# Kernel tuning notes

Measured on AMD Instinct MI355X. Metric: run time of the kernel, lower is better.

## Reference

```python
import jax, jax.numpy as jnp
import numpy as np

K, A, DIM = 1024, 16384, 512


def setup_inputs() -> dict:
    key = jax.random.key(0)
    ks = jax.random.split(key, 8)
    B, H, W = 2048, 8, 8
    z_t = jax.random.randint(ks[0], (B, H, W), 0, K, dtype=jnp.int64)
    z_tp1 = jax.random.randint(ks[1], (B, H, W), 0, K, dtype=jnp.int64)
    embed_w = jax.random.normal(ks[2], (K, DIM), dtype=jnp.float32) * 0.02
    # MLP: Linear(2*dim -> dim), GELU, Linear(dim -> dim)
    lim1 = 1.0 / np.sqrt(2 * DIM)
    w1 = jax.random.uniform(ks[3], (2 * DIM, DIM), minval=-lim1, maxval=lim1, dtype=jnp.float32)
    b1 = jax.random.uniform(ks[4], (DIM,), minval=-lim1, maxval=lim1, dtype=jnp.float32)
    lim2 = 1.0 / np.sqrt(DIM)
    w2 = jax.random.uniform(ks[5], (DIM, DIM), minval=-lim2, maxval=lim2, dtype=jnp.float32)
    b2 = jax.random.uniform(ks[6], (DIM,), minval=-lim2, maxval=lim2, dtype=jnp.float32)
    codebook_w = jax.random.normal(ks[7], (A, DIM), dtype=jnp.float32) * 0.02
    return {"z_t": z_t, "z_tp1": z_tp1, "embed_w": embed_w, "w1": w1, "b1": b1,
            "w2": w2, "b2": b2, "codebook_w": codebook_w}


def reference(z_t, z_tp1, embed_w, w1, b1, w2, b2, codebook_w):
    B = z_t.shape[0]
    # embed int code grids and mean-pool over H*W tokens -> [B, dim]
    e_t = embed_w[z_t.reshape(B, -1)].mean(axis=1)
    e_tp1 = embed_w[z_tp1.reshape(B, -1)].mean(axis=1)
    h = jnp.concatenate([e_t, e_tp1], axis=-1)          # [B, 2*dim]
    h = jax.nn.gelu(h @ w1 + b1, approximate=False)
    e = h @ w2 + b2                                      # [B, dim]
    # VQ: squared L2 distance to each code, argmin, gather
    d2 = (jnp.sum(e * e, axis=1, keepdims=True)
          - 2.0 * e @ codebook_w.T
          + jnp.sum(codebook_w * codebook_w, axis=1)[None, :])  # [B, A]
    ids = jnp.argmin(d2, axis=1)                         # [B]
    q = codebook_w[ids]                                  # [B, dim]
    return ids, q
```

## Files before the change

### kernel.cpp

```cpp
#include <hip/hip_runtime.h>
#include <hip/hip_bf16.h>

#define TOK 64
#define DIMC 512

typedef __attribute__((ext_vector_type(8))) short v8s;
typedef __attribute__((ext_vector_type(4))) float v4f;

#define MFMA16 __builtin_amdgcn_mfma_f32_16x16x32_bf16

__device__ __forceinline__ unsigned int f2ord(float f) {
  unsigned int u = __float_as_uint(f);
  return (u & 0x80000000u) ? ~u : (u | 0x80000000u);
}

__device__ __forceinline__ float gelu_exact(float x) {
  return 0.5f * x * (1.0f + erff(x * 0.70710678118654752440f));
}

__device__ __forceinline__ unsigned short f2bf(float x) {
  unsigned int u = __float_as_uint(x);
  return (unsigned short)((u + 0x7FFFu + ((u >> 16) & 1u)) >> 16);
}
__device__ __forceinline__ float bf2f(unsigned short h) {
  return __uint_as_float((unsigned int)h << 16);
}

__device__ __forceinline__ void gl2lds16(const void* g, void* l) {
  __builtin_amdgcn_global_load_lds((const __attribute__((address_space(1))) void*)g,
                                   (__attribute__((address_space(3))) void*)l,
                                   16, 0, 0);
}

__global__ __launch_bounds__(256) void k_prep(
    const int* __restrict__ zt, const int* __restrict__ ztp,
    const float* __restrict__ emb,
    unsigned short* __restrict__ hh, unsigned short* __restrict__ hl,
    unsigned long long* __restrict__ rowmin,
    const float* __restrict__ w1, unsigned short* __restrict__ w1th,
    unsigned short* __restrict__ w1tl,
    const float* __restrict__ w2, unsigned short* __restrict__ w2th,
    unsigned short* __restrict__ w2tl,
    const float* __restrict__ cb, unsigned short* __restrict__ ch,
    unsigned short* __restrict__ cl, float* __restrict__ cnorm) {
  __shared__ int codes[128];
  __shared__ float tbuf[32][33];
  const int bid = blockIdx.x;
  const int tid = threadIdx.x;

  if (bid < 2048) {
    const int b = bid;
    if (tid < 64) codes[tid] = zt[b * TOK + tid];
    else if (tid < 128) codes[tid] = ztp[b * TOK + (tid - 64)];
    if (tid == 0) rowmin[b] = 0xFFFFFFFFFFFFFFFFull;
    __syncthreads();
    const int half = tid >> 7;
    const int c4 = tid & 127;
    const float4* emb4 = (const float4*)emb;
    float4 s = make_float4(0.f, 0.f, 0.f, 0.f);
    #pragma unroll 8
    for (int t = 0; t < TOK; t++) {
      const int code = codes[half * TOK + t];
      const float4 v = emb4[code * 128 + c4];
      s.x += v.x; s.y += v.y; s.z += v.z; s.w += v.w;
    }
    const float inv = 1.0f / 64.0f;
    float f[4] = {s.x * inv, s.y * inv, s.z * inv, s.w * inv};
    unsigned short hi[4], lo[4];
    #pragma unroll
    for (int i = 0; i < 4; i++) {
      hi[i] = f2bf(f[i]);
      lo[i] = f2bf(f[i] - bf2f(hi[i]));
    }
    const int off = b * 1024 + half * 512 + c4 * 4;
    *(ushort4*)&hh[off] = make_ushort4(hi[0], hi[1], hi[2], hi[3]);
    *(ushort4*)&hl[off] = make_ushort4(lo[0], lo[1], lo[2], lo[3]);
  } else if (bid < 2816) {
    const float* w; unsigned short *wth, *wtl; int Kd, N, k0, n0;
    if (bid < 2560) {
      const int i = bid - 2048;
      w = w1; wth = w1th; wtl = w1tl; Kd = 1024; N = 512;
      k0 = (i & 31) * 32; n0 = (i >> 5) * 32;
    } else {
      const int i = bid - 2560;
      w = w2; wth = w2th; wtl = w2tl; Kd = 512; N = 512;
      k0 = (i & 15) * 32; n0 = (i >> 4) * 32;
    }
    const int c = tid & 31, r = tid >> 5;
    #pragma unroll
    for (int i = 0; i < 4; i++)
      tbuf[r + i * 8][c] = w[(size_t)(k0 + r + i * 8) * N + n0 + c];
    __syncthreads();
    #pragma unroll
    for (int i = 0; i < 4; i++) {
      const float v = tbuf[c][r + i * 8];
      const unsigned short hi = f2bf(v);
      const unsigned short lo = f2bf(v - bf2f(hi));
      wth[(size_t)(n0 + r + i * 8) * Kd + k0 + c] = hi;
      wtl[(size_t)(n0 + r + i * 8) * Kd + k0 + c] = lo;
    }
  } else {
    const int row = (bid - 2816) * 4 + (tid >> 6);
    const int lane = tid & 63;
    const float4* cb4 = (const float4*)cb;
    const float4 va = cb4[row * 128 + lane * 2];
    const float4 vb = cb4[row * 128 + lane * 2 + 1];
    float s = va.x * va.x + va.y * va.y + va.z * va.z + va.w * va.w
            + vb.x * vb.x + vb.y * vb.y + vb.z * vb.z + vb.w * vb.w;
    float f[8] = {va.x, va.y, va.z, va.w, vb.x, vb.y, vb.z, vb.w};
    unsigned short hi[8], lo[8];
    #pragma unroll
    for (int i = 0; i < 8; i++) {
      hi[i] = f2bf(f[i]);
      lo[i] = f2bf(f[i] - bf2f(hi[i]));
    }
    ushort4* chp = (ushort4*)&ch[row * DIMC + lane * 8];
    ushort4* clp = (ushort4*)&cl[row * DIMC + lane * 8];
    chp[0] = make_ushort4(hi[0], hi[1], hi[2], hi[3]);
    chp[1] = make_ushort4(hi[4], hi[5], hi[6], hi[7]);
    clp[0] = make_ushort4(lo[0], lo[1], lo[2], lo[3]);
    clp[1] = make_ushort4(lo[4], lo[5], lo[6], lo[7]);
    #pragma unroll
    for (int off = 32; off > 0; off >>= 1) s += __shfl_down(s, off);
    if (lane == 0) cnorm[row] = s;
  }
}

template <bool GELU>
__global__ __launch_bounds__(256) void k_gemm(const unsigned short* __restrict__ Ah_,
                                              const unsigned short* __restrict__ Al_,
                                              const unsigned short* __restrict__ Bh_,
                                              const unsigned short* __restrict__ Bl_,
                                              const float* __restrict__ bias,
                                              unsigned short* __restrict__ oh,
                                              unsigned short* __restrict__ ol,
                                              int Kd, int N) {
  __shared__ unsigned short AhS[2][2048];
  __shared__ unsigned short AlS[2][2048];
  __shared__ unsigned short BhS[2][4096];
  __shared__ unsigned short BlS[2][4096];

  const int tid = threadIdx.x;
  const int lane = tid & 63;
  const int wid = tid >> 6;
  const int m0 = blockIdx.x * 32;
  const int n0 = blockIdx.y * 64;

  const unsigned short* Ab_h = Ah_ + (size_t)m0 * Kd;
  const unsigned short* Ab_l = Al_ + (size_t)m0 * Kd;
  const unsigned short* Bb_h = Bh_ + (size_t)n0 * Kd;
  const unsigned short* Bb_l = Bl_ + (size_t)n0 * Kd;

  const int srow = lane >> 2;
  const int sk = ((lane & 3) ^ ((lane >> 3) & 3)) * 8;
  const int wm = wid >> 1, wn = wid & 1;
  const int fr = lane & 15;
  const int q = lane >> 4;
  const int fqs = (q ^ ((fr >> 1) & 3)) * 8;

  v4f acc[2];
  acc[0] = (v4f)(0.f);
  acc[1] = (v4f)(0.f);

  auto stage = [&](int b, int k0) {
    #pragma unroll
    for (int u = 0; u < 6; u++) {
      const int i = wid * 6 + u;
      const unsigned short* gs; unsigned short* ls; int slab, seg, rstride;
      if (i < 4)       { gs = Ab_h; ls = AhS[b]; slab = i >> 1;         seg = i & 1;         rstride = 1024; }
      else if (i < 8)  { gs = Ab_l; ls = AlS[b]; slab = (i - 4) >> 1;   seg = (i - 4) & 1;   rstride = 1024; }
      else if (i < 16) { gs = Bb_h; ls = BhS[b]; slab = (i - 8) >> 2;   seg = (i - 8) & 3;   rstride = 2048; }
      else             { gs = Bb_l; ls = BlS[b]; slab = (i - 16) >> 2;  seg = (i - 16) & 3;  rstride = 2048; }
      gl2lds16(gs + (size_t)(seg * 16 + srow) * Kd + k0 + slab * 32 + sk,
               ls + slab * rstride + seg * 512);
    }
  };

  stage(0, 0);
  int cur = 0;
  for (int k0 = 0; k0 < Kd; k0 += 64) {
    __syncthreads();
    if (k0 + 64 < Kd) stage(cur ^ 1, k0 + 64);

    #pragma unroll
    for (int kk = 0; kk < 2; kk++) {
      const int ar = kk * 1024 + (wm * 16 + fr) * 32 + fqs;
      const v8s ah = *(const v8s*)&AhS[cur][ar];
      const v8s al = *(const v8s*)&AlS[cur][ar];
      #pragma unroll
      for (int nt = 0; nt < 2; nt++) {
        const int br = kk * 2048 + (wn * 32 + nt * 16 + fr) * 32 + fqs;
        const v8s bh = *(const v8s*)&BhS[cur][br];
        const v8s bl = *(const v8s*)&BlS[cur][br];
        acc[nt] = MFMA16(ah, bh, acc[nt], 0, 0, 0);
        acc[nt] = MFMA16(ah, bl, acc[nt], 0, 0, 0);
        acc[nt] = MFMA16(al, bh, acc[nt], 0, 0, 0);
      }
    }
    cur ^= 1;
  }

  const int col16 = lane & 15;
  #pragma unroll
  for (int nt = 0; nt < 2; nt++) {
    const int col = n0 + wn * 32 + nt * 16 + col16;
    const float bv = bias[col];
    #pragma unroll
    for (int reg = 0; reg < 4; reg++) {
      const int row = m0 + wm * 16 + q * 4 + reg;
      float v = acc[nt][reg] + bv;
      if (GELU) v = gelu_exact(v);
      const unsigned short hi = f2bf(v);
      oh[(size_t)row * N + col] = hi;
      ol[(size_t)row * N + col] = f2bf(v - bf2f(hi));
    }
  }
}

__global__ __launch_bounds__(512, 2) void k_vq(const unsigned short* __restrict__ eh,
                                               const unsigned short* __restrict__ el,
                                               const unsigned short* __restrict__ ch,
                                               const unsigned short* __restrict__ cl,
                                               const float* __restrict__ cnorm,
                                               unsigned long long* __restrict__ rowmin) {
  __shared__ unsigned short lds[2 * 32768];

  const int tid = threadIdx.x;
  const int lane = tid & 63;
  const int wid = tid >> 6;
  const int bid = blockIdx.x;
  const int x = (bid >> 3) & 7;
  const int y = (((bid >> 6) & 7) << 3) | (bid & 7);
  const int r0 = x * 256;
  const int c0 = y * 256;

  const unsigned short* ehB = eh + (size_t)r0 * DIMC;
  const unsigned short* elB = el + (size_t)r0 * DIMC;
  const unsigned short* chB = ch + (size_t)c0 * DIMC;
  const unsigned short* clB = cl + (size_t)c0 * DIMC;

  const int srow = lane >> 2;
  const int sk = ((lane & 3) ^ ((lane >> 3) & 3)) * 8;
  const int wm = wid >> 1;
  const int wn = wid & 1;
  const int fr = lane & 15;
  const int q = lane >> 4;
  const int fqs = (q ^ ((fr >> 1) & 3)) * 8;

  v4f acc[4][8];
  #pragma unroll
  for (int i = 0; i < 4; i++)
    #pragma unroll
    for (int jj = 0; jj < 8; jj++) acc[i][jj] = (v4f)(0.f);

  const unsigned short* gp[8];
  int lo_[8];
  #pragma unroll
  for (int u = 0; u < 8; u++) {
    const int i = wid * 8 + u;
    const unsigned short* gs; int off, rbase;
    if (i < 16)      { gs = ehB; off = 0;     rbase = i * 16; }
    else if (i < 32) { gs = elB; off = 8192;  rbase = (i - 16) * 16; }
    else if (i < 48) { gs = chB; off = 16384; rbase = (i - 32) * 16; }
    else             { gs = clB; off = 24576; rbase = (i - 48) * 16; }
    gp[u] = gs + (size_t)(rbase + srow) * DIMC + sk;
    lo_[u] = off + rbase * 32;
  }

  auto stage = [&](int buf, int k0) {
    #pragma unroll
    for (int u = 0; u < 8; u++)
      gl2lds16(gp[u] + k0, lds + buf * 32768 + lo_[u]);
  };

  stage(0, 0);
  __syncthreads();

  for (int t = 0; t < 16; ++t) {
    if (t < 15) stage((t + 1) & 1, (t + 1) * 32);

    const unsigned short* base = lds + (t & 1) * 32768;
    v8s ah[4], al[4];
    #pragma unroll
    for (int mt = 0; mt < 4; mt++) {
      const int ar = (wm * 64 + mt * 16 + fr) * 32 + fqs;
      ah[mt] = *(const v8s*)&base[ar];
      al[mt] = *(const v8s*)&base[8192 + ar];
    }
    __builtin_amdgcn_s_setprio(1);
    #pragma unroll
    for (int nt = 0; nt < 8; nt++) {
      const int br = (wn * 128 + nt * 16 + fr) * 32 + fqs;
      const v8s bh = *(const v8s*)&base[16384 + br];
      const v8s bl = *(const v8s*)&base[24576 + br];
      #pragma unroll
      for (int mt = 0; mt < 4; mt++) {
        acc[mt][nt] = MFMA16(ah[mt], bh, acc[mt][nt], 0, 0, 0);
        acc[mt][nt] = MFMA16(ah[mt], bl, acc[mt][nt], 0, 0, 0);
        acc[mt][nt] = MFMA16(al[mt], bh, acc[mt][nt], 0, 0, 0);
      }
    }
    __builtin_amdgcn_s_setprio(0);
    if (t < 15) __syncthreads();
  }

  const int col16 = lane & 15;
  float cn[8];
  #pragma unroll
  for (int nt = 0; nt < 8; nt++) cn[nt] = cnorm[c0 + wn * 128 + nt * 16 + col16];

  #pragma unroll
  for (int mt = 0; mt < 4; mt++) {
    #pragma unroll
    for (int reg = 0; reg < 4; reg++) {
      const int row = r0 + wm * 64 + mt * 16 + q * 4 + reg;
      float best = fmaf(-2.f, acc[mt][0][reg], cn[0]);
      int bid2 = c0 + wn * 128 + col16;
      #pragma unroll
      for (int nt = 1; nt < 8; nt++) {
        const float s = fmaf(-2.f, acc[mt][nt][reg], cn[nt]);
        const int id = c0 + wn * 128 + nt * 16 + col16;
        if (s < best) { best = s; bid2 = id; }
      }
      unsigned long long v =
          ((unsigned long long)f2ord(best) << 32) | (unsigned int)bid2;
      #pragma unroll
      for (int off = 8; off > 0; off >>= 1) {
        const unsigned long long o = __shfl_down(v, off, 16);
        if (o < v) v = o;
      }
      if (col16 == 0) atomicMin(&rowmin[row], v);
    }
  }
}

__global__ __launch_bounds__(64) void k_final(const unsigned long long* __restrict__ rowmin,
                                              const float* __restrict__ cb,
                                              float* __restrict__ out,
                                              int B) {
  const int b = blockIdx.x;
  const int t = threadIdx.x;
  const unsigned long long m = rowmin[b];
  const int id = (int)(unsigned int)(m & 0xFFFFFFFFull);
  if (t == 0) out[b] = (float)id;
  float4* q4 = (float4*)(out + B) + b * 128;
  const float4* cb4 = (const float4*)cb + (size_t)id * 128;
  q4[t] = cb4[t];
  q4[t + 64] = cb4[t + 64];
}

extern "C" void kernel_launch(void* const* d_in, const int* in_sizes, int n_in,
                              void* d_out, int out_size, void* d_ws, size_t ws_size,
                              hipStream_t stream) {
  const int* zt = (const int*)d_in[0];
  const int* ztp = (const int*)d_in[1];
  const float* emb = (const float*)d_in[2];
  const float* w1 = (const float*)d_in[3];
  const float* b1 = (const float*)d_in[4];
  const float* w2 = (const float*)d_in[5];
  const float* b2 = (const float*)d_in[6];
  const float* cb = (const float*)d_in[7];
  float* out = (float*)d_out;

  const int B = in_sizes[0] / TOK;
  const int A = in_sizes[7] / DIMC;

  char* p = (char*)d_ws;
  unsigned short* hh = (unsigned short*)p;  p += (size_t)B * 1024 * 2;
  unsigned short* hl = (unsigned short*)p;  p += (size_t)B * 1024 * 2;
  unsigned short* w1th = (unsigned short*)p; p += (size_t)512 * 1024 * 2;
  unsigned short* w1tl = (unsigned short*)p; p += (size_t)512 * 1024 * 2;
  unsigned short* w2th = (unsigned short*)p; p += (size_t)512 * 512 * 2;
  unsigned short* w2tl = (unsigned short*)p; p += (size_t)512 * 512 * 2;
  unsigned short* h1h = (unsigned short*)p; p += (size_t)B * DIMC * 2;
  unsigned short* h1l = (unsigned short*)p; p += (size_t)B * DIMC * 2;
  unsigned short* eh = (unsigned short*)p;  p += (size_t)B * DIMC * 2;
  unsigned short* el = (unsigned short*)p;  p += (size_t)B * DIMC * 2;
  unsigned short* ch = (unsigned short*)p;  p += (size_t)A * DIMC * 2;
  unsigned short* cl = (unsigned short*)p;  p += (size_t)A * DIMC * 2;
  float* cnorm = (float*)p;                 p += (size_t)A * 4;
  unsigned long long* rowmin = (unsigned long long*)p;

  k_prep<<<2816 + A / 4, 256, 0, stream>>>(zt, ztp, emb, hh, hl, rowmin,
                                           w1, w1th, w1tl, w2, w2th, w2tl,
                                           cb, ch, cl, cnorm);
  k_gemm<true><<<dim3(B / 32, 512 / 64), 256, 0, stream>>>(hh, hl, w1th, w1tl, b1, h1h, h1l, 1024, 512);
  k_gemm<false><<<dim3(B / 32, 512 / 64), 256, 0, stream>>>(h1h, h1l, w2th, w2tl, b2, eh, el, 512, 512);
  k_vq<<<(B / 256) * (A / 256), 512, 0, stream>>>(eh, el, ch, cl, cnorm, rowmin);
  k_final<<<B, 64, 0, stream>>>(rowmin, cb, out, B);
}
```

Measured before the change: 222.0 us.

## Move w2 and codebook prep into GEMM1 launch to overlap independent work

Takes the w2 transpose/split and the codebook bf16 split and norm computation out of the prep kernel and runs them as extra blocks of the first GEMM launch. Those blocks then overlap with GEMM1 compute instead of lengthening the critical prep stage. GEMM2 is specialized with constant dimensions, and the final gather packs four rows per 256-thread block. It adds branchy heterogeneous blocks and a larger grid for GEMM1, and GEMM2 declares unused shared arrays that the compiler should drop.

```diff
diff --git a/kernel.cpp b/kernel.cpp
--- a/kernel.cpp
+++ b/kernel.cpp
@@ -38,11 +38,7 @@
     unsigned short* __restrict__ hh, unsigned short* __restrict__ hl,
     unsigned long long* __restrict__ rowmin,
     const float* __restrict__ w1, unsigned short* __restrict__ w1th,
-    unsigned short* __restrict__ w1tl,
-    const float* __restrict__ w2, unsigned short* __restrict__ w2th,
-    unsigned short* __restrict__ w2tl,
-    const float* __restrict__ cb, unsigned short* __restrict__ ch,
-    unsigned short* __restrict__ cl, float* __restrict__ cnorm) {
+    unsigned short* __restrict__ w1tl) {
   __shared__ int codes[128];
   __shared__ float tbuf[32][33];
   const int bid = blockIdx.x;
@@ -75,32 +71,134 @@
     const int off = b * 1024 + half * 512 + c4 * 4;
     *(ushort4*)&hh[off] = make_ushort4(hi[0], hi[1], hi[2], hi[3]);
     *(ushort4*)&hl[off] = make_ushort4(lo[0], lo[1], lo[2], lo[3]);
-  } else if (bid < 2816) {
-    const float* w; unsigned short *wth, *wtl; int Kd, N, k0, n0;
-    if (bid < 2560) {
-      const int i = bid - 2048;
-      w = w1; wth = w1th; wtl = w1tl; Kd = 1024; N = 512;
-      k0 = (i & 31) * 32; n0 = (i >> 5) * 32;
-    } else {
-      const int i = bid - 2560;
-      w = w2; wth = w2th; wtl = w2tl; Kd = 512; N = 512;
-      k0 = (i & 15) * 32; n0 = (i >> 4) * 32;
-    }
+  } else {
+    const int i = bid - 2048;
+    const int Kd = 1024, N = 512;
+    const int k0 = (i & 31) * 32, n0 = (i >> 5) * 32;
     const int c = tid & 31, r = tid >> 5;
     #pragma unroll
-    for (int i = 0; i < 4; i++)
-      tbuf[r + i * 8][c] = w[(size_t)(k0 + r + i * 8) * N + n0 + c];
+    for (int j = 0; j < 4; j++)
+      tbuf[r + j * 8][c] = w1[(size_t)(k0 + r + j * 8) * N + n0 + c];
     __syncthreads();
     #pragma unroll
-    for (int i = 0; i < 4; i++) {
-      const float v = tbuf[c][r + i * 8];
+    for (int j = 0; j < 4; j++) {
+      const float v = tbuf[c][r + j * 8];
       const unsigned short hi = f2bf(v);
       const unsigned short lo = f2bf(v - bf2f(hi));
-      wth[(size_t)(n0 + r + i * 8) * Kd + k0 + c] = hi;
-      wtl[(size_t)(n0 + r + i * 8) * Kd + k0 + c] = lo;
+      w1th[(size_t)(n0 + r + j * 8) * Kd + k0 + c] = hi;
+      w1tl[(size_t)(n0 + r + j * 8) * Kd + k0 + c] = lo;
+    }
+  }
+}
+
+__global__ __launch_bounds__(256) void k_gemm1_fused(
+    const unsigned short* __restrict__ Ah_, const unsigned short* __restrict__ Al_,
+    const unsigned short* __restrict__ Bh_, const unsigned short* __restrict__ Bl_,
+    const float* __restrict__ bias,
+    unsigned short* __restrict__ oh, unsigned short* __restrict__ ol,
+    const float* __restrict__ w2, unsigned short* __restrict__ w2th,
+    unsigned short* __restrict__ w2tl,
+    const float* __restrict__ cb, unsigned short* __restrict__ ch,
+    unsigned short* __restrict__ cl, float* __restrict__ cnorm) {
+  __shared__ unsigned short smem[24576];
+  const int bid = blockIdx.x;
+  const int tid = threadIdx.x;
+
+  if (bid < 512) {
+    const int Kd = 1024, N = 512;
+    const int lane = tid & 63;
+    const int wid = tid >> 6;
+    const int m0 = (bid & 63) * 32;
+    const int n0 = (bid >> 6) * 64;
+
+    const unsigned short* Ab_h = Ah_ + (size_t)m0 * Kd;
+    const unsigned short* Ab_l = Al_ + (size_t)m0 * Kd;
+    const unsigned short* Bb_h = Bh_ + (size_t)n0 * Kd;
+    const unsigned short* Bb_l = Bl_ + (size_t)n0 * Kd;
+
+    const int srow = lane >> 2;
+    const int sk = ((lane & 3) ^ ((lane >> 3) & 3)) * 8;
+    const int wm = wid >> 1, wn = wid & 1;
+    const int fr = lane & 15;
+    const int q = lane >> 4;
+    const int fqs = (q ^ ((fr >> 1) & 3)) * 8;
+
+    v4f acc[2];
+    acc[0] = (v4f)(0.f);
+    acc[1] = (v4f)(0.f);
+
+    auto stage = [&](int b, int k0) {
+      #pragma unroll
+      for (int u = 0; u < 6; u++) {
+        const int i = wid * 6 + u;
+        const unsigned short* gs; unsigned short* ls; int slab, seg, rstride;
+        if (i < 4)       { gs = Ab_h; ls = smem + b * 2048;          slab = i >> 1;        seg = i & 1;        rstride = 1024; }
+        else if (i < 8)  { gs = Ab_l; ls = smem + 4096 + b * 2048;   slab = (i - 4) >> 1;  seg = (i - 4) & 1;  rstride = 1024; }
+        else if (i < 16) { gs = Bb_h; ls = smem + 8192 + b * 4096;   slab = (i - 8) >> 2;  seg = (i - 8) & 3;  rstride = 2048; }
+        else             { gs = Bb_l; ls = smem + 16384 + b * 4096;  slab = (i - 16) >> 2; seg = (i - 16) & 3; rstride = 2048; }
+        gl2lds16(gs + (size_t)(seg * 16 + srow) * Kd + k0 + slab * 32 + sk,
+                 ls + slab * rstride + seg * 512);
+      }
+    };
+
+    stage(0, 0);
+    int cur = 0;
+    for (int k0 = 0; k0 < Kd; k0 += 64) {
+      __syncthreads();
+      if (k0 + 64 < Kd) stage(cur ^ 1, k0 + 64);
+
+      #pragma unroll
+      for (int kk = 0; kk < 2; kk++) {
+        const int ar = kk * 1024 + (wm * 16 + fr) * 32 + fqs;
+        const v8s ah = *(const v8s*)&smem[cur * 2048 + ar];
+        const v8s al = *(const v8s*)&smem[4096 + cur * 2048 + ar];
+        #pragma unroll
+        for (int nt = 0; nt < 2; nt++) {
+          const int br = kk * 2048 + (wn * 32 + nt * 16 + fr) * 32 + fqs;
+          const v8s bh = *(const v8s*)&smem[8192 + cur * 4096 + br];
+          const v8s bl = *(const v8s*)&smem[16384 + cur * 4096 + br];
+          acc[nt] = MFMA16(ah, bh, acc[nt], 0, 0, 0);
+          acc[nt] = MFMA16(ah, bl, acc[nt], 0, 0, 0);
+          acc[nt] = MFMA16(al, bh, acc[nt], 0, 0, 0);
+        }
+      }
+      cur ^= 1;
+    }
+
+    const int col16 = lane & 15;
+    #pragma unroll
+    for (int nt = 0; nt < 2; nt++) {
+      const int col = n0 + wn * 32 + nt * 16 + col16;
+      const float bv = bias[col];
+      #pragma unroll
+      for (int reg = 0; reg < 4; reg++) {
+        const int row = m0 + wm * 16 + q * 4 + reg;
+        float v = acc[nt][reg] + bv;
+        v = gelu_exact(v);
+        const unsigned short hi = f2bf(v);
+        oh[(size_t)row * N + col] = hi;
+        ol[(size_t)row * N + col] = f2bf(v - bf2f(hi));
+      }
+    }
+  } else if (bid < 768) {
+    const int i = bid - 512;
+    const int k0 = (i & 15) * 32, n0 = (i >> 4) * 32;
+    float* tbuf = (float*)smem;
+    const int c = tid & 31, r = tid >> 5;
+    #pragma unroll
+    for (int j = 0; j < 4; j++)
+      tbuf[(r + j * 8) * 33 + c] = w2[(size_t)(k0 + r + j * 8) * 512 + n0 + c];
+    __syncthreads();
+    #pragma unroll
+    for (int j = 0; j < 4; j++) {
+      const float v = tbuf[c * 33 + r + j * 8];
+      const unsigned short hi = f2bf(v);
+      const unsigned short lo = f2bf(v - bf2f(hi));
+      w2th[(size_t)(n0 + r + j * 8) * 512 + k0 + c] = hi;
+      w2tl[(size_t)(n0 + r + j * 8) * 512 + k0 + c] = lo;
     }
   } else {
-    const int row = (bid - 2816) * 4 + (tid >> 6);
+    const int row = (bid - 768) * 4 + (tid >> 6);
     const int lane = tid & 63;
     const float4* cb4 = (const float4*)cb;
     const float4 va = cb4[row * 128 + lane * 2];
@@ -126,20 +224,21 @@
   }
 }
 
-template <bool GELU>
-__global__ __launch_bounds__(256) void k_gemm(const unsigned short* __restrict__ Ah_,
-                                              const unsigned short* __restrict__ Al_,
-                                              const unsigned short* __restrict__ Bh_,
-                                              const unsigned short* __restrict__ Bl_,
-                                              const float* __restrict__ bias,
-                                              unsigned short* __restrict__ oh,
-                                              unsigned short* __restrict__ ol,
-                                              int Kd, int N) {
-  __shared__ unsigned short AhS[2][2048];
-  __shared__ unsigned short AlS[2][2048];
-  __shared__ unsigned short BhS[2][4096];
-  __shared__ unsigned short BlS[2][4096];
-
+__global__ __launch_bounds__(256) void k_gemm2(const unsigned short* __restrict__ Ah_,
+                                               const unsigned short* __restrict__ Al_,
+                                               const unsigned short* __restrict__ Bh_,
+                                               const unsigned short* __restrict__ Bl_,
+                                               const float* __restrict__ bias,
+                                               unsigned short* __restrict__ oh,
+                                               unsigned short* __restrict__ ol) {
+  __shared__ unsigned short AhS[2][1024];
+  __shared__ unsigned short AlS[2][1024];
+  __shared__ unsigned short BhS[2][2048];
+  __shared__ unsigned short BlS[2][2048];
+  (void)AhS; (void)AlS; (void)BhS; (void)BlS;
+  __shared__ unsigned short smem[24576];
+
+  const int Kd = 512, N = 512;
   const int tid = threadIdx.x;
   const int lane = tid & 63;
   const int wid = tid >> 6;
@@ -167,10 +266,10 @@
     for (int u = 0; u < 6; u++) {
       const int i = wid * 6 + u;
       const unsigned short* gs; unsigned short* ls; int slab, seg, rstride;
-      if (i < 4)       { gs = Ab_h; ls = AhS[b]; slab = i >> 1;         seg = i & 1;         rstride = 1024; }
-      else if (i < 8)  { gs = Ab_l; ls = AlS[b]; slab = (i - 4) >> 1;   seg = (i - 4) & 1;   rstride = 1024; }
-      else if (i < 16) { gs = Bb_h; ls = BhS[b]; slab = (i - 8) >> 2;   seg = (i - 8) & 3;   rstride = 2048; }
-      else             { gs = Bb_l; ls = BlS[b]; slab = (i - 16) >> 2;  seg = (i - 16) & 3;  rstride = 2048; }
+      if (i < 4)       { gs = Ab_h; ls = smem + b * 2048;          slab = i >> 1;        seg = i & 1;        rstride = 1024; }
+      else if (i < 8)  { gs = Ab_l; ls = smem + 4096 + b * 2048;   slab = (i - 4) >> 1;  seg = (i - 4) & 1;  rstride = 1024; }
+      else if (i < 16) { gs = Bb_h; ls = smem + 8192 + b * 4096;   slab = (i - 8) >> 2;  seg = (i - 8) & 3;  rstride = 2048; }
+      else             { gs = Bb_l; ls = smem + 16384 + b * 4096;  slab = (i - 16) >> 2; seg = (i - 16) & 3; rstride = 2048; }
       gl2lds16(gs + (size_t)(seg * 16 + srow) * Kd + k0 + slab * 32 + sk,
                ls + slab * rstride + seg * 512);
     }
@@ -185,13 +284,13 @@
     #pragma unroll
     for (int kk = 0; kk < 2; kk++) {
       const int ar = kk * 1024 + (wm * 16 + fr) * 32 + fqs;
-      const v8s ah = *(const v8s*)&AhS[cur][ar];
-      const v8s al = *(const v8s*)&AlS[cur][ar];
+      const v8s ah = *(const v8s*)&smem[cur * 2048 + ar];
+      const v8s al = *(const v8s*)&smem[4096 + cur * 2048 + ar];
       #pragma unroll
       for (int nt = 0; nt < 2; nt++) {
         const int br = kk * 2048 + (wn * 32 + nt * 16 + fr) * 32 + fqs;
-        const v8s bh = *(const v8s*)&BhS[cur][br];
-        const v8s bl = *(const v8s*)&BlS[cur][br];
+        const v8s bh = *(const v8s*)&smem[8192 + cur * 4096 + br];
+        const v8s bl = *(const v8s*)&smem[16384 + cur * 4096 + br];
         acc[nt] = MFMA16(ah, bh, acc[nt], 0, 0, 0);
         acc[nt] = MFMA16(ah, bl, acc[nt], 0, 0, 0);
         acc[nt] = MFMA16(al, bh, acc[nt], 0, 0, 0);
@@ -209,7 +308,6 @@
     for (int reg = 0; reg < 4; reg++) {
       const int row = m0 + wm * 16 + q * 4 + reg;
       float v = acc[nt][reg] + bv;
-      if (GELU) v = gelu_exact(v);
       const unsigned short hi = f2bf(v);
       oh[(size_t)row * N + col] = hi;
       ol[(size_t)row * N + col] = f2bf(v - bf2f(hi));
@@ -334,12 +432,12 @@
   }
 }
 
-__global__ __launch_bounds__(64) void k_final(const unsigned long long* __restrict__ rowmin,
-                                              const float* __restrict__ cb,
-                                              float* __restrict__ out,
-                                              int B) {
-  const int b = blockIdx.x;
-  const int t = threadIdx.x;
+__global__ __launch_bounds__(256) void k_final(const unsigned long long* __restrict__ rowmin,
+                                               const float* __restrict__ cb,
+                                               float* __restrict__ out,
+                                               int B) {
+  const int b = blockIdx.x * 4 + (threadIdx.x >> 6);
+  const int t = threadIdx.x & 63;
   const unsigned long long m = rowmin[b];
   const int id = (int)(unsigned int)(m & 0xFFFFFFFFull);
   if (t == 0) out[b] = (float)id;
@@ -381,11 +479,10 @@
   float* cnorm = (float*)p;                 p += (size_t)A * 4;
   unsigned long long* rowmin = (unsigned long long*)p;
 
-  k_prep<<<2816 + A / 4, 256, 0, stream>>>(zt, ztp, emb, hh, hl, rowmin,
-                                           w1, w1th, w1tl, w2, w2th, w2tl,
-                                           cb, ch, cl, cnorm);
-  k_gemm<true><<<dim3(B / 32, 512 / 64), 256, 0, stream>>>(hh, hl, w1th, w1tl, b1, h1h, h1l, 1024, 512);
-  k_gemm<false><<<dim3(B / 32, 512 / 64), 256, 0, stream>>>(h1h, h1l, w2th, w2tl, b2, eh, el, 512, 512);
+  k_prep<<<2560, 256, 0, stream>>>(zt, ztp, emb, hh, hl, rowmin, w1, w1th, w1tl);
+  k_gemm1_fused<<<768 + A / 4, 256, 0, stream>>>(hh, hl, w1th, w1tl, b1, h1h, h1l,
+                                                 w2, w2th, w2tl, cb, ch, cl, cnorm);
+  k_gemm2<<<dim3(B / 32, 512 / 64), 256, 0, stream>>>(h1h, h1l, w2th, w2tl, b2, eh, el);
   k_vq<<<(B / 256) * (A / 256), 512, 0, stream>>>(eh, el, ch, cl, cnorm, rowmin);
-  k_final<<<B, 64, 0, stream>>>(rowmin, cb, out, B);
-}
+  k_final<<<B / 4, 256, 0, stream>>>(rowmin, cb, out, B);
+}
```

Result: faster. 216.6 us (-2.4%).
